# Optimization experiments

Hardware: AMD Instinct MI355X
Metric: run time of the kernel (lower is better)

The kernel has to match this reference:

```python
import jax, jax.numpy as jnp
import numpy as np

# Static conv hyperparameters (match init_kwargs)
STRIDE = (1, 1)
PAD = (1, 1)
DIL = (1, 1)
GROUPS = 1
DG = 1  # num_deformable_groups


def setup_inputs() -> dict:
    key = jax.random.key(0)
    k1, k2, k3 = jax.random.split(key, 3)
    B, C, H, W = 4, 256, 64, 64
    OC, kh, kw = 256, 3, 3
    x = jax.random.normal(k1, (B, C, H, W), dtype=jnp.float32)
    # offset: [B, DG*2*kh*kw, Ho, Wo], ordered (tap, [dy, dx]) per deformable group
    offset = jax.random.normal(k2, (B, DG * 2 * kh * kw, H, W), dtype=jnp.float32)
    n = C * kh * kw
    stdv = 1.0 / np.sqrt(n)
    weight = jax.random.uniform(k3, (OC, C // GROUPS, kh, kw), dtype=jnp.float32,
                                minval=-stdv, maxval=stdv)
    return {"x": x, "offset": offset, "weight": weight}


def _deform_conv(x, offset, weight):
    B, C, H, W = x.shape
    OC, Cg_w, kh, kw = weight.shape
    sh, sw = STRIDE
    ph, pw = PAD
    dh, dw = DIL
    Ho = (H + 2 * ph - (dh * (kh - 1) + 1)) // sh + 1
    Wo = (W + 2 * pw - (dw * (kw - 1) + 1)) // sw + 1
    K = kh * kw
    Cg = C // DG  # channels per deformable group

    # offsets: [B, DG, K, 2, Ho, Wo]; channel 0 = dy (h), channel 1 = dx (w)
    off = offset.reshape(B, DG, K, 2, Ho, Wo)

    # base (undeformed) sampling positions per tap
    ki, kj = jnp.meshgrid(jnp.arange(kh), jnp.arange(kw), indexing='ij')
    base_h = (jnp.arange(Ho) * sh - ph)[None, :] + (ki.reshape(-1) * dh)[:, None]  # [K, Ho]
    base_w = (jnp.arange(Wo) * sw - pw)[None, :] + (kj.reshape(-1) * dw)[:, None]  # [K, Wo]

    pos_h = base_h[None, None, :, :, None].astype(x.dtype) + off[:, :, :, 0]  # [B,DG,K,Ho,Wo]
    pos_w = base_w[None, None, :, None, :].astype(x.dtype) + off[:, :, :, 1]  # [B,DG,K,Ho,Wo]

    h0f = jnp.floor(pos_h)
    w0f = jnp.floor(pos_w)
    lh = pos_h - h0f  # fractional parts
    lw = pos_w - w0f
    h0 = h0f.astype(jnp.int32)
    w0 = w0f.astype(jnp.int32)

    xg = x.reshape(B, DG, Cg, H * W)

    def gather(hi, wi):
        # zero-padded gather: out-of-range corners contribute 0 (mmcv DCNv1 semantics)
        valid = (hi >= 0) & (hi < H) & (wi >= 0) & (wi < W)  # [B,DG,K,Ho,Wo]
        idx = jnp.clip(hi, 0, H - 1) * W + jnp.clip(wi, 0, W - 1)
        flat = idx.reshape(B, DG, 1, K * Ho * Wo)
        vals = jnp.take_along_axis(
            xg, jnp.broadcast_to(flat, (B, DG, Cg, K * Ho * Wo)), axis=3)
        vals = vals.reshape(B, DG, Cg, K, Ho, Wo)
        return vals * valid[:, :, None].astype(x.dtype)

    # bilinear interpolation over 4 corners -> im2col columns [B,DG,Cg,K,Ho,Wo]
    cols = (gather(h0, w0) * ((1 - lh) * (1 - lw))[:, :, None]
            + gather(h0, w0 + 1) * ((1 - lh) * lw)[:, :, None]
            + gather(h0 + 1, w0) * (lh * (1 - lw))[:, :, None]
            + gather(h0 + 1, w0 + 1) * (lh * lw)[:, :, None])

    # grouped GEMM: columns x weight
    cols = cols.reshape(B, GROUPS, C // GROUPS, K, Ho, Wo)
    wg = weight.reshape(GROUPS, OC // GROUPS, Cg_w, K)
    out = jnp.einsum('gock,bgckhw->bgohw', wg, cols)
    return out.reshape(B, OC, Ho, Wo)


def reference(x, offset, weight):
    return _deform_conv(x, offset, weight)
```

## Files before the change

kernel.cpp:

```cpp
#include <hip/hip_runtime.h>
#include <hip/hip_bf16.h>
#include <math.h>


constexpr int B  = 4;
constexpr int C  = 256;
constexpr int H  = 64;
constexpr int W  = 64;
constexpr int OC = 256;
constexpr int Ho = 64;
constexpr int Wo = 64;

constexpr int NT     = 64;
constexpr int CHUNKS = 72;
constexpr int WROW   = 40;

constexpr size_t WA_ELTS  = (size_t)CHUNKS * OC * WROW;
constexpr size_t XB_ELTS  = (size_t)B * 8 * 4096 * 32;
constexpr size_t OUT_ELTS = (size_t)B * OC * Ho * Wo;

typedef __attribute__((ext_vector_type(8))) short bf16x8;
typedef __attribute__((ext_vector_type(4))) float f32x4;

__device__ __forceinline__ float bf_lo(unsigned u) {
    union { unsigned i; float f; } c; c.i = u << 16; return c.f;
}
__device__ __forceinline__ float bf_hi(unsigned u) {
    union { unsigned i; float f; } c; c.i = u & 0xffff0000u; return c.f;
}
__device__ __forceinline__ ushort fbf(float f) {
    __hip_bfloat16 h = __float2bfloat16(f); return *(ushort*)&h;
}

__global__ __launch_bounds__(256)
void prep_all(const float* __restrict__ x, const float* __restrict__ wt,
              ushort* __restrict__ xb, ushort* __restrict__ wA)
{
    __shared__ ushort sx[128 * WROW];
    __shared__ ushort sw[CHUNKS * WROW];
    const int t = threadIdx.x;

    if (blockIdx.x < 1024) {
        const int blk = blockIdx.x;
        const int hwb = blk & 31;
        const int cb  = (blk >> 5) & 7;
        const int b   = blk >> 8;
        const int hw0 = hwb << 7;
        const int lhw = t & 127, chalf = t >> 7;
        #pragma unroll
        for (int i = 0; i < 16; ++i) {
            const int c = i * 2 + chalf;
            sx[lhw * WROW + c] =
                fbf(x[(((size_t)(b * 256 + cb * 32 + c)) << 12) + hw0 + lhw]);
        }
        __syncthreads();
        const int whw = t >> 1, wh = t & 1;
        const uint4 v0 = *(const uint4*)&sx[whw * WROW + wh * 16];
        const uint4 v1 = *(const uint4*)&sx[whw * WROW + wh * 16 + 8];
        uint4* dst = (uint4*)(xb + ((size_t)((b * 8 + cb) * 4096 + hw0) << 5));
        dst[whw * 4 + wh * 2 + 0] = v0;
        dst[whw * 4 + wh * 2 + 1] = v1;
    } else {
        const int oc = blockIdx.x - 1024;
        const int c  = t, chb = c >> 5, kk = c & 31;
        const float* wp = wt + ((size_t)oc * C + c) * 9;
        #pragma unroll
        for (int tap = 0; tap < 9; ++tap)
            sw[(tap * 8 + chb) * WROW + kk] = fbf(wp[tap]);
        if (c < CHUNKS) {
            #pragma unroll
            for (int j = 0; j < 8; ++j) sw[c * WROW + 32 + j] = 0;
        }
        __syncthreads();
        const uint4* sv = (const uint4*)sw;
        for (int i = c; i < CHUNKS * 5; i += 256) {
            const int row = i / 5, q = i % 5;
            ((uint4*)(wA + ((size_t)row * OC + oc) * WROW))[q] = sv[i];
        }
    }
}

__global__ __launch_bounds__(512, 1)
void dcn_mfma(const ushort* __restrict__ xb, const float* __restrict__ off,
              const ushort* __restrict__ wA_g, float* __restrict__ po)
{
    __shared__ __align__(16) ushort s_wA[OC * WROW];
    __shared__ __align__(16) ushort s_col[NT * WROW];
    __shared__ int2   s_midx[9 * NT];
    __shared__ float4 s_mw[9 * NT];

    const int xcd = blockIdx.x & 7;
    const int ii  = blockIdx.x >> 3;
    const int b   = xcd & 3;
    const int khalf = ii & 1;
    const int ho  = ((xcd >> 2) << 5) + (ii >> 1);
    const int ch0 = khalf * 36, ch1 = ch0 + 36;
    float* outp = po + (size_t)khalf * OUT_ELTS;
    const int tid = threadIdx.x;

    for (int s = tid; s < 9 * NT; s += 512) {
        const int n   = s & 63;
        const int tap = s >> 6;
        const float dy = off[((size_t)(b * 18 + 2 * tap)     * Ho + ho) * Wo + n];
        const float dx = off[((size_t)(b * 18 + 2 * tap + 1) * Ho + ho) * Wo + n];
        const float ph = (float)(ho - 1 + tap / 3) + dy;
        const float pw = (float)(n  - 1 + tap % 3) + dx;
        const float h0f = floorf(ph), w0f = floorf(pw);
        const int h0 = (int)h0f, w0 = (int)w0f;
        const float lh = ph - h0f, lw = pw - w0f;
        const int wb = min(max(w0, 0), W - 2);
        const int ht = min(max(h0, 0), H - 1);
        const int hb = min(max(h0 + 1, 0), H - 1);
        const float s0 = (wb == w0) ? (1.f - lw) : ((wb == w0 + 1) ? lw : 0.f);
        const float s1 = (wb + 1 == w0 + 1) ? lw : ((wb + 1 == w0) ? (1.f - lw) : 0.f);
        const float wtp = (h0 >= 0 && h0 < H)         ? (1.f - lh) : 0.f;
        const float wbt = (h0 + 1 >= 0 && h0 + 1 < H) ? lh         : 0.f;
        s_midx[s] = make_int2(ht * W + wb, hb * W + wb);
        s_mw[s]   = make_float4(wtp * s0, wtp * s1, wbt * s0, wbt * s1);
    }

    const int lane = tid & 63;
    const int wv   = tid >> 6;
    const int ocb  = wv >> 1;
    const int phh  = wv & 1;
    const int kq   = lane >> 4;
    const int mr   = lane & 15;

    const int sm_tid = tid - 256;
    const int sn  = sm_tid >> 2;
    const int sgg = sm_tid & 3;

    f32x4 acc[4][2];
    #pragma unroll
    for (int mt = 0; mt < 4; ++mt)
        #pragma unroll
        for (int nt = 0; nt < 2; ++nt)
            acc[mt][nt] = (f32x4){0.f, 0.f, 0.f, 0.f};

    for (int ch = ch0; ch < ch1; ++ch) {
        __syncthreads();

        if (tid < 256) {
            #pragma unroll
            for (int i = 0; i < 5; ++i) {
                const int seg = wv * 5 + i;
                __builtin_amdgcn_global_load_lds(
                    (const __attribute__((address_space(1))) void*)
                        (wA_g + (size_t)ch * OC * WROW + seg * 512 + lane * 8),
                    (__attribute__((address_space(3))) void*)&s_wA[seg * 512],
                    16, 0, 0);
            }
        } else {
            const int tap = ch >> 3;
            const int cb  = ch & 7;
            const int2   mi = s_midx[tap * NT + sn];
            const float4 mw = s_mw[tap * NT + sn];
            const ushort* xp = xb + ((size_t)(b * 8 + cb) << 17) + (sgg << 3);
            const uint4 c00 = *(const uint4*)(xp + ((size_t)mi.x << 5));
            const uint4 c01 = *(const uint4*)(xp + (((size_t)mi.x + 1) << 5));
            const uint4 c10 = *(const uint4*)(xp + ((size_t)mi.y << 5));
            const uint4 c11 = *(const uint4*)(xp + (((size_t)mi.y + 1) << 5));
            union { ushort pk[8]; uint4 v; } u;
            const unsigned a00[4] = {c00.x, c00.y, c00.z, c00.w};
            const unsigned a01[4] = {c01.x, c01.y, c01.z, c01.w};
            const unsigned a10[4] = {c10.x, c10.y, c10.z, c10.w};
            const unsigned a11[4] = {c11.x, c11.y, c11.z, c11.w};
            #pragma unroll
            for (int j = 0; j < 4; ++j) {
                const float vlo = mw.x * bf_lo(a00[j]) + mw.y * bf_lo(a01[j])
                                + mw.z * bf_lo(a10[j]) + mw.w * bf_lo(a11[j]);
                const float vhi = mw.x * bf_hi(a00[j]) + mw.y * bf_hi(a01[j])
                                + mw.z * bf_hi(a10[j]) + mw.w * bf_hi(a11[j]);
                u.pk[2 * j]     = fbf(vlo);
                u.pk[2 * j + 1] = fbf(vhi);
            }
            *(uint4*)&s_col[sn * WROW + sgg * 8] = u.v;
        }
        __syncthreads();

        bf16x8 bfr[2];
        #pragma unroll
        for (int nt = 0; nt < 2; ++nt)
            bfr[nt] = *(const bf16x8*)&s_col[((phh * 2 + nt) * 16 + mr) * WROW + kq * 8];
        #pragma unroll
        for (int mt = 0; mt < 4; ++mt) {
            const bf16x8 afr = *(const bf16x8*)&s_wA[(ocb * 64 + mt * 16 + mr) * WROW + kq * 8];
            #pragma unroll
            for (int nt = 0; nt < 2; ++nt)
                acc[mt][nt] = __builtin_amdgcn_mfma_f32_16x16x32_bf16(afr, bfr[nt], acc[mt][nt], 0, 0, 0);
        }
    }

    #pragma unroll
    for (int mt = 0; mt < 4; ++mt)
        #pragma unroll
        for (int nt = 0; nt < 2; ++nt)
            #pragma unroll
            for (int r = 0; r < 4; ++r) {
                const int oc = ocb * 64 + mt * 16 + kq * 4 + r;
                const int wo = (phh * 2 + nt) * 16 + mr;
                outp[((size_t)(b * OC + oc) * Ho + ho) * Wo + wo] = acc[mt][nt][r];
            }
}

__global__ __launch_bounds__(256)
void reduce2(const float4* __restrict__ p0, const float4* __restrict__ p1,
             float4* __restrict__ out)
{
    const int i = blockIdx.x * 256 + threadIdx.x;
    const float4 a = p0[i], b = p1[i];
    out[i] = make_float4(a.x + b.x, a.y + b.y, a.z + b.z, a.w + b.w);
}

extern "C" void kernel_launch(void* const* d_in, const int* in_sizes, int n_in,
                              void* d_out, int out_size, void* d_ws, size_t ws_size,
                              hipStream_t stream)
{
    const float* x   = (const float*)d_in[0];
    const float* off = (const float*)d_in[1];
    const float* wt  = (const float*)d_in[2];
    float* out = (float*)d_out;

    ushort* wA = (ushort*)d_ws;
    ushort* xb = wA + WA_ELTS;
    float*  po = (float*)(xb + XB_ELTS);

    prep_all<<<1280, 256, 0, stream>>>(x, wt, xb, wA);
    dcn_mfma<<<512, 512, 0, stream>>>(xb, off, wA, po);
    reduce2<<<(int)(OUT_ELTS / 4 / 256), 256, 0, stream>>>(
        (const float4*)po, (const float4*)(po + OUT_ELTS), (float4*)out);
}
```

Measured before the change: 121.8 us.

## Fuse split-K reduction into GEMM kernel via last-arriver atomic flags

Drops the separate reduce2 launch. Each block writes its partial sum, increments a per-(batch,row) counter, and the second block to finish adds the other half's partial to its accumulators and writes the final output. The flags are reset inside prep_all. This saves a kernel launch and a full read/write pass over the output. The cost is threadfences, atomics and a serial dependency between paired blocks. The first finisher still writes its partial to global memory.

```diff
diff --git a/kernel.cpp b/kernel.cpp
--- a/kernel.cpp
+++ b/kernel.cpp
@@ -34,7 +34,8 @@
 
 __global__ __launch_bounds__(256)
 void prep_all(const float* __restrict__ x, const float* __restrict__ wt,
-              ushort* __restrict__ xb, ushort* __restrict__ wA)
+              ushort* __restrict__ xb, ushort* __restrict__ wA,
+              int* __restrict__ flags)
 {
     __shared__ ushort sx[128 * WROW];
     __shared__ ushort sw[CHUNKS * WROW];
@@ -61,6 +62,7 @@
         dst[whw * 4 + wh * 2 + 0] = v0;
         dst[whw * 4 + wh * 2 + 1] = v1;
     } else {
+        if (blockIdx.x == 1024) flags[t] = 0;
         const int oc = blockIdx.x - 1024;
         const int c  = t, chb = c >> 5, kk = c & 31;
         const float* wp = wt + ((size_t)oc * C + c) * 9;
@@ -82,12 +84,14 @@
 
 __global__ __launch_bounds__(512, 1)
 void dcn_mfma(const ushort* __restrict__ xb, const float* __restrict__ off,
-              const ushort* __restrict__ wA_g, float* __restrict__ po)
+              const ushort* __restrict__ wA_g, float* __restrict__ po,
+              int* __restrict__ flags, float* __restrict__ out)
 {
     __shared__ __align__(16) ushort s_wA[OC * WROW];
     __shared__ __align__(16) ushort s_col[NT * WROW];
     __shared__ int2   s_midx[9 * NT];
     __shared__ float4 s_mw[9 * NT];
+    __shared__ int    s_last;
 
     const int xcd = blockIdx.x & 7;
     const int ii  = blockIdx.x >> 3;
@@ -201,15 +205,26 @@
                 const int wo = (phh * 2 + nt) * 16 + mr;
                 outp[((size_t)(b * OC + oc) * Ho + ho) * Wo + wo] = acc[mt][nt][r];
             }
-}
-
-__global__ __launch_bounds__(256)
-void reduce2(const float4* __restrict__ p0, const float4* __restrict__ p1,
-             float4* __restrict__ out)
-{
-    const int i = blockIdx.x * 256 + threadIdx.x;
-    const float4 a = p0[i], b = p1[i];
-    out[i] = make_float4(a.x + b.x, a.y + b.y, a.z + b.z, a.w + b.w);
+
+    __threadfence();
+    __syncthreads();
+    if (tid == 0) s_last = atomicAdd(&flags[b * 64 + ho], 1);
+    __syncthreads();
+    if (s_last == 1) {
+        __threadfence();
+        const float* pp = po + (size_t)(khalf ^ 1) * OUT_ELTS;
+        #pragma unroll
+        for (int mt = 0; mt < 4; ++mt)
+            #pragma unroll
+            for (int nt = 0; nt < 2; ++nt)
+                #pragma unroll
+                for (int r = 0; r < 4; ++r) {
+                    const int oc = ocb * 64 + mt * 16 + kq * 4 + r;
+                    const int wo = (phh * 2 + nt) * 16 + mr;
+                    const size_t idx = ((size_t)(b * OC + oc) * Ho + ho) * Wo + wo;
+                    out[idx] = acc[mt][nt][r] + pp[idx];
+                }
+    }
 }
 
 extern "C" void kernel_launch(void* const* d_in, const int* in_sizes, int n_in,
@@ -224,9 +239,8 @@
     ushort* wA = (ushort*)d_ws;
     ushort* xb = wA + WA_ELTS;
     float*  po = (float*)(xb + XB_ELTS);
-
-    prep_all<<<1280, 256, 0, stream>>>(x, wt, xb, wA);
-    dcn_mfma<<<512, 512, 0, stream>>>(xb, off, wA, po);
-    reduce2<<<(int)(OUT_ELTS / 4 / 256), 256, 0, stream>>>(
-        (const float4*)po, (const float4*)(po + OUT_ELTS), (float4*)out);
-}
+    int* flags = (int*)(po + 2 * OUT_ELTS);
+
+    prep_all<<<1280, 256, 0, stream>>>(x, wt, xb, wA, flags);
+    dcn_mfma<<<512, 512, 0, stream>>>(xb, off, wA, po, flags, out);
+}
```

Result: slower. 289.7 us (+137.8%).
